# Kernel tuning notes

Measured on AMD Instinct MI355X. Metric: run time of the kernel, lower is better.

The kernel has to match this reference:

```python
import jax, jax.numpy as jnp
import numpy as np

N = 8192
IN_F = 128
OUT_F = 128


def setup_inputs() -> dict:
    key = jax.random.key(0)
    k1, k2, k3, k4 = jax.random.split(key, 4)
    h = jax.random.normal(k1, (N, IN_F), dtype=jnp.float32)
    pos = jax.random.normal(k2, (N, 1, 3), dtype=jnp.float32)
    # xavier_uniform-ish scale for params
    W = jax.random.uniform(k3, (IN_F, OUT_F), dtype=jnp.float32,
                           minval=-1.0, maxval=1.0) * (1.414 * np.sqrt(6.0 / (IN_F + OUT_F)))
    a = jax.random.uniform(k4, (2 * OUT_F + 3, 1), dtype=jnp.float32,
                           minval=-1.0, maxval=1.0) * (1.414 * np.sqrt(6.0 / (2 * OUT_F + 3 + 1)))
    return {"h": h, "pos": pos, "W": W, "a": a}


def reference(h, pos, W, a):
    # Wh: [N, F]
    Wh = h @ W
    F_ = Wh.shape[1]
    a1 = a[:F_, 0]          # weights on Wh[j] (the repeated / neighbor features)
    a2 = a[F_:2 * F_, 0]    # weights on Wh[i] (the repeat_interleaved / center features)
    a3 = a[2 * F_:, 0]      # weights on pos[i] - pos[j]
    p = pos.reshape(-1, 3)  # [N, 3]
    s_j = Wh @ a1           # [N]
    s_i = Wh @ a2           # [N]
    p_a = p @ a3            # [N]
    # e[i, j] = leaky_relu(Wh[j].a1 + Wh[i].a2 + (pos[i]-pos[j]).a3)
    e = jax.nn.leaky_relu(s_i[:, None] + s_j[None, :] + p_a[:, None] - p_a[None, :],
                          negative_slope=0.2)  # [N, N]
    attention = jax.nn.softmax(e, axis=1)
    # eval mode: dropout is identity
    h_prime = attention @ Wh  # [N, F]
    return jax.nn.elu(h_prime)
```

## Files before the change

### kernel.cpp

```cpp
#include <hip/hip_runtime.h>
#include <hip/hip_bf16.h>

#define N 8192
#define F 128
#define JC 4
#define JSLICE (N / JC)

typedef __attribute__((ext_vector_type(4)))  float f32x4;
typedef __attribute__((ext_vector_type(16))) float f32x16;
typedef __attribute__((ext_vector_type(8)))  short short8;

static __device__ __forceinline__ short bf16bits(float x) {
  __hip_bfloat16 b = __float2bfloat16(x);
  return *reinterpret_cast<short*>(&b);
}

__global__ __launch_bounds__(256) void k_gemm_cd(
    const float* __restrict__ h, const float* __restrict__ pos,
    const float* __restrict__ W, const float* __restrict__ a,
    unsigned short* __restrict__ WhTf, float* __restrict__ cArr,
    float* __restrict__ dArr)
{
  __shared__ float Ws[128 * 128];
  const int tid = threadIdx.x;
  const int r0  = blockIdx.x * 16;

  {
    f32x4* Ws4 = (f32x4*)Ws;
    const f32x4* Wg4 = (const f32x4*)W;
#pragma unroll
    for (int q = 0; q < 16; ++q) Ws4[q * 256 + tid] = Wg4[q * 256 + tid];
  }
  __syncthreads();

  const int rg  = tid >> 5;
  const int c32 = tid & 31;

  f32x4 acc0, acc1;
#pragma unroll
  for (int i = 0; i < 4; ++i) { acc0[i] = 0.0f; acc1[i] = 0.0f; }

  const f32x4* h40 = (const f32x4*)(h + (size_t)(r0 + rg * 2) * 128);
  const f32x4* h41 = (const f32x4*)(h + (size_t)(r0 + rg * 2 + 1) * 128);
  const f32x4* Ws4 = (const f32x4*)Ws;

#pragma unroll 4
  for (int k4 = 0; k4 < 32; ++k4) {
    f32x4 hv0 = h40[k4];
    f32x4 hv1 = h41[k4];
#pragma unroll
    for (int e = 0; e < 4; ++e) {
      f32x4 w = Ws4[(k4 * 4 + e) * 32 + c32];
      acc0 += hv0[e] * w;
      acc1 += hv1[e] * w;
    }
  }

  f32x4 a1v = *(const f32x4*)(a + c32 * 4);
  f32x4 a2v = *(const f32x4*)(a + 128 + c32 * 4);
#pragma unroll
  for (int rr = 0; rr < 2; ++rr) {
    f32x4 accR = rr ? acc1 : acc0;
    f32x4 t1 = accR * a1v;
    f32x4 t2 = accR * a2v;
    float s1 = t1[0] + t1[1] + t1[2] + t1[3];
    float s2 = t2[0] + t2[1] + t2[2] + t2[3];
#pragma unroll
    for (int m = 1; m < 32; m <<= 1) {
      s1 += __shfl_xor(s1, m);
      s2 += __shfl_xor(s2, m);
    }
    if (c32 == 0) {
      const int row = r0 + rg * 2 + rr;
      float pa = pos[row * 3 + 0] * a[256] + pos[row * 3 + 1] * a[257] +
                 pos[row * 3 + 2] * a[258];
      cArr[row] = s2 + pa;
      dArr[row] = s1 - pa;
    }
  }

  __syncthreads();
  float* tmp = Ws;
  {
    const int base = (rg * 2) * 132 + c32 * 4;
    *(f32x4*)&tmp[base]       = acc0;
    *(f32x4*)&tmp[base + 132] = acc1;
  }
  __syncthreads();
  {
    const int col  = tid >> 1;
    const int half = tid & 1;
    short8 o;
#pragma unroll
    for (int rr = 0; rr < 8; ++rr)
      o[rr] = bf16bits(tmp[(half * 8 + rr) * 132 + col]);
    *(short8*)(WhTf + (size_t)(r0 >> 4) * 2048 + col * 16 + half * 8) = o;
  }
}

__global__ __launch_bounds__(256, 2) void k_flash(
    const unsigned short* __restrict__ WhTf, const float* __restrict__ cArr,
    const float* __restrict__ dArr, float* __restrict__ pnum,
    float* __restrict__ pden)
{
  __shared__ __align__(16) float dS[JSLICE];
  __shared__ float redA[64 * 128];
  __shared__ float redB[64 * 128];
  __shared__ float denA[64];
  __shared__ float denB[64];

  const int tid = threadIdx.x;
  const int jc  = blockIdx.x >> 7;
  const int r0  = (blockIdx.x & 127) * 64;

  {
    const f32x4* s4 = (const f32x4*)(dArr + (size_t)jc * JSLICE);
    f32x4* t4 = (f32x4*)dS;
    t4[tid]       = s4[tid];
    t4[256 + tid] = s4[256 + tid];
  }
  __syncthreads();

  const int w  = tid >> 6;
  const int l  = tid & 63;
  const int cl = l & 31;
  const int kh = l >> 5;
  const int jw = w * (JSLICE / 4);
  const float L2E = 1.44269504f;
  const float ci0 = cArr[r0 + cl] * L2E;
  const float ci1 = cArr[r0 + 32 + cl] * L2E;

  f32x16 acc[2][4];
#pragma unroll
  for (int R = 0; R < 2; ++R)
#pragma unroll
    for (int G = 0; G < 4; ++G)
#pragma unroll
      for (int i = 0; i < 16; ++i) acc[R][G][i] = 0.0f;

  float den0 = 0.0f, den1 = 0.0f;

  const unsigned short* bPtr =
      WhTf + ((size_t)(jc * JSLICE + jw) >> 4) * 2048 + cl * 16 + kh * 8;
  const float* dPtr = dS + jw + kh * 8;

  short8 b0 = *(const short8*)(bPtr);
  short8 b1 = *(const short8*)(bPtr + 512);
  short8 b2 = *(const short8*)(bPtr + 1024);
  short8 b3 = *(const short8*)(bPtr + 1536);
  f32x4 dj0 = *(const f32x4*)(dPtr);
  f32x4 dj1 = *(const f32x4*)(dPtr + 4);
  bPtr += 2048; dPtr += 16;

  const int iters = (JSLICE / 4) / 16;
  for (int kk = 0; kk < iters; ++kk) {
    short8 n0 = *(const short8*)(bPtr);
    short8 n1 = *(const short8*)(bPtr + 512);
    short8 n2 = *(const short8*)(bPtr + 1024);
    short8 n3 = *(const short8*)(bPtr + 1536);
    f32x4 nd0 = *(const f32x4*)(dPtr);
    f32x4 nd1 = *(const f32x4*)(dPtr + 4);

    float p0[8], p1[8];
#pragma unroll
    for (int e = 0; e < 8; ++e) {
      float dj = (e < 4) ? dj0[e] : dj1[e - 4];
      float u0 = __builtin_fmaf(dj, L2E, ci0);
      u0 = fmaxf(u0, 0.2f * u0);
      float pv0 = __builtin_amdgcn_exp2f(u0);
      den0 += pv0; p0[e] = pv0;
      float u1 = __builtin_fmaf(dj, L2E, ci1);
      u1 = fmaxf(u1, 0.2f * u1);
      float pv1 = __builtin_amdgcn_exp2f(u1);
      den1 += pv1; p1[e] = pv1;
    }
    short8 af0, af1;
#pragma unroll
    for (int e = 0; e < 8; ++e) { af0[e] = bf16bits(p0[e]); af1[e] = bf16bits(p1[e]); }

    acc[0][0] = __builtin_amdgcn_mfma_f32_32x32x16_bf16(af0, b0, acc[0][0], 0, 0, 0);
    acc[1][0] = __builtin_amdgcn_mfma_f32_32x32x16_bf16(af1, b0, acc[1][0], 0, 0, 0);
    acc[0][1] = __builtin_amdgcn_mfma_f32_32x32x16_bf16(af0, b1, acc[0][1], 0, 0, 0);
    acc[1][1] = __builtin_amdgcn_mfma_f32_32x32x16_bf16(af1, b1, acc[1][1], 0, 0, 0);
    acc[0][2] = __builtin_amdgcn_mfma_f32_32x32x16_bf16(af0, b2, acc[0][2], 0, 0, 0);
    acc[1][2] = __builtin_amdgcn_mfma_f32_32x32x16_bf16(af1, b2, acc[1][2], 0, 0, 0);
    acc[0][3] = __builtin_amdgcn_mfma_f32_32x32x16_bf16(af0, b3, acc[0][3], 0, 0, 0);
    acc[1][3] = __builtin_amdgcn_mfma_f32_32x32x16_bf16(af1, b3, acc[1][3], 0, 0, 0);

    b0 = n0; b1 = n1; b2 = n2; b3 = n3;
    dj0 = nd0; dj1 = nd1;
    bPtr += 2048; dPtr += 16;
  }

  den0 += __shfl_xor(den0, 32);
  den1 += __shfl_xor(den1, 32);

  float* redW = (w & 1) ? redB : redA;
  float* denW = (w & 1) ? denB : denA;
  const int rhi = 4 * kh;
  if (w < 2) {
#pragma unroll
    for (int reg = 0; reg < 16; ++reg) {
      const int rt = (reg & 3) + 8 * (reg >> 2) + rhi;
#pragma unroll
      for (int R = 0; R < 2; ++R)
#pragma unroll
        for (int G = 0; G < 4; ++G)
          redW[(R * 32 + rt) * 128 + G * 32 + cl] = acc[R][G][reg];
    }
    if (l < 32) { denW[cl] = den0; denW[32 + cl] = den1; }
  }
  __syncthreads();
  if (w >= 2) {
#pragma unroll
    for (int reg = 0; reg < 16; ++reg) {
      const int rt = (reg & 3) + 8 * (reg >> 2) + rhi;
#pragma unroll
      for (int R = 0; R < 2; ++R)
#pragma unroll
        for (int G = 0; G < 4; ++G)
          redW[(R * 32 + rt) * 128 + G * 32 + cl] += acc[R][G][reg];
    }
    if (l < 32) { denW[cl] += den0; denW[32 + cl] += den1; }
  }
  __syncthreads();

  {
    f32x4* pn4 = (f32x4*)(pnum + (size_t)jc * N * F + (size_t)r0 * 128);
    const f32x4* rA = (const f32x4*)redA;
    const f32x4* rB = (const f32x4*)redB;
#pragma unroll
    for (int q = 0; q < 8; ++q)
      pn4[q * 256 + tid] = rA[q * 256 + tid] + rB[q * 256 + tid];
    if (tid < 64) pden[(size_t)jc * N + r0 + tid] = denA[tid] + denB[tid];
  }
}

__global__ __launch_bounds__(256) void k_final(
    const float* __restrict__ pnum, const float* __restrict__ pden,
    float* __restrict__ out)
{
  const int g = blockIdx.x * 256 + threadIdx.x;
  const int row = g >> 5;
  f32x4 n;
#pragma unroll
  for (int i = 0; i < 4; ++i) n[i] = 0.0f;
  float dd = 0.0f;
#pragma unroll
  for (int c = 0; c < JC; ++c) {
    n += ((const f32x4*)pnum)[(size_t)c * (N * F / 4) + g];
    dd += pden[(size_t)c * N + row];
  }
  f32x4 r = n * (1.0f / dd);
#pragma unroll
  for (int i = 0; i < 4; ++i) {
    float x = r[i];
    r[i] = x > 0.0f ? x : (__builtin_amdgcn_exp2f(x * 1.44269504f) - 1.0f);
  }
  ((f32x4*)out)[g] = r;
}

extern "C" void kernel_launch(void* const* d_in, const int* in_sizes, int n_in,
                              void* d_out, int out_size, void* d_ws, size_t ws_size,
                              hipStream_t stream)
{
  const float* h   = (const float*)d_in[0];
  const float* pos = (const float*)d_in[1];
  const float* W   = (const float*)d_in[2];
  const float* a   = (const float*)d_in[3];
  float* out = (float*)d_out;

  char* ws = (char*)d_ws;
  unsigned short* WhTf = (unsigned short*)ws;
  float* cArr = (float*)(ws + (size_t)2 * 1024 * 1024);
  float* dArr = cArr + N;
  float* pden = dArr + N;
  float* pnum = pden + (size_t)JC * N;

  hipLaunchKernelGGL(k_gemm_cd, dim3(512), dim3(256), 0, stream,
                     h, pos, W, a, WhTf, cArr, dArr);
  hipLaunchKernelGGL(k_flash, dim3(128 * JC), dim3(256), 0, stream,
                     WhTf, cArr, dArr, pnum, pden);
  hipLaunchKernelGGL(k_final, dim3((N * F / 4) / 256), dim3(256), 0, stream,
                     pnum, pden, out);
}
```

Before: 115.3 us.

## Split flash kernel work per wave by row tile and raise occupancy

Result: faster. 111.1 us (-3.7%).

```diff
diff --git a/kernel.cpp b/kernel.cpp
--- a/kernel.cpp
+++ b/kernel.cpp
@@ -3,7 +3,7 @@
 
 #define N 8192
 #define F 128
-#define JC 4
+#define JC 8
 #define JSLICE (N / JC)
 
 typedef __attribute__((ext_vector_type(4)))  float f32x4;
@@ -98,16 +98,14 @@
   }
 }
 
-__global__ __launch_bounds__(256, 2) void k_flash(
+__global__ __launch_bounds__(256, 4) void k_flash(
     const unsigned short* __restrict__ WhTf, const float* __restrict__ cArr,
     const float* __restrict__ dArr, float* __restrict__ pnum,
     float* __restrict__ pden)
 {
   __shared__ __align__(16) float dS[JSLICE];
-  __shared__ float redA[64 * 128];
-  __shared__ float redB[64 * 128];
-  __shared__ float denA[64];
-  __shared__ float denB[64];
+  __shared__ float red[64 * 128];
+  __shared__ float denS[64];
 
   const int tid = threadIdx.x;
   const int jc  = blockIdx.x >> 7;
@@ -115,9 +113,7 @@
 
   {
     const f32x4* s4 = (const f32x4*)(dArr + (size_t)jc * JSLICE);
-    f32x4* t4 = (f32x4*)dS;
-    t4[tid]       = s4[tid];
-    t4[256 + tid] = s4[256 + tid];
+    ((f32x4*)dS)[tid] = s4[tid];
   }
   __syncthreads();
 
@@ -125,20 +121,15 @@
   const int l  = tid & 63;
   const int cl = l & 31;
   const int kh = l >> 5;
-  const int jw = w * (JSLICE / 4);
+  const int rt = w & 1;
+  const int jw = (w >> 1) * (JSLICE / 2);
   const float L2E = 1.44269504f;
-  const float ci0 = cArr[r0 + cl] * L2E;
-  const float ci1 = cArr[r0 + 32 + cl] * L2E;
-
-  f32x16 acc[2][4];
-#pragma unroll
-  for (int R = 0; R < 2; ++R)
-#pragma unroll
-    for (int G = 0; G < 4; ++G)
-#pragma unroll
-      for (int i = 0; i < 16; ++i) acc[R][G][i] = 0.0f;
-
-  float den0 = 0.0f, den1 = 0.0f;
+  const float ci = cArr[r0 + rt * 32 + cl] * L2E;
+
+  f32x16 acc0, acc1, acc2, acc3;
+#pragma unroll
+  for (int i = 0; i < 16; ++i) { acc0[i] = 0; acc1[i] = 0; acc2[i] = 0; acc3[i] = 0; }
+  float den = 0.0f;
 
   const unsigned short* bPtr =
       WhTf + ((size_t)(jc * JSLICE + jw) >> 4) * 2048 + cl * 16 + kh * 8;
@@ -148,91 +139,72 @@
   short8 b1 = *(const short8*)(bPtr + 512);
   short8 b2 = *(const short8*)(bPtr + 1024);
   short8 b3 = *(const short8*)(bPtr + 1536);
-  f32x4 dj0 = *(const f32x4*)(dPtr);
-  f32x4 dj1 = *(const f32x4*)(dPtr + 4);
-  bPtr += 2048; dPtr += 16;
-
-  const int iters = (JSLICE / 4) / 16;
+  bPtr += 2048;
+
+  const int iters = (JSLICE / 2) / 16;
   for (int kk = 0; kk < iters; ++kk) {
     short8 n0 = *(const short8*)(bPtr);
     short8 n1 = *(const short8*)(bPtr + 512);
     short8 n2 = *(const short8*)(bPtr + 1024);
     short8 n3 = *(const short8*)(bPtr + 1536);
-    f32x4 nd0 = *(const f32x4*)(dPtr);
-    f32x4 nd1 = *(const f32x4*)(dPtr + 4);
-
-    float p0[8], p1[8];
+
+    f32x4 dj0 = *(const f32x4*)(dPtr);
+    f32x4 dj1 = *(const f32x4*)(dPtr + 4);
+    short8 af;
 #pragma unroll
     for (int e = 0; e < 8; ++e) {
       float dj = (e < 4) ? dj0[e] : dj1[e - 4];
-      float u0 = __builtin_fmaf(dj, L2E, ci0);
-      u0 = fmaxf(u0, 0.2f * u0);
-      float pv0 = __builtin_amdgcn_exp2f(u0);
-      den0 += pv0; p0[e] = pv0;
-      float u1 = __builtin_fmaf(dj, L2E, ci1);
-      u1 = fmaxf(u1, 0.2f * u1);
-      float pv1 = __builtin_amdgcn_exp2f(u1);
-      den1 += pv1; p1[e] = pv1;
-    }
-    short8 af0, af1;
-#pragma unroll
-    for (int e = 0; e < 8; ++e) { af0[e] = bf16bits(p0[e]); af1[e] = bf16bits(p1[e]); }
-
-    acc[0][0] = __builtin_amdgcn_mfma_f32_32x32x16_bf16(af0, b0, acc[0][0], 0, 0, 0);
-    acc[1][0] = __builtin_amdgcn_mfma_f32_32x32x16_bf16(af1, b0, acc[1][0], 0, 0, 0);
-    acc[0][1] = __builtin_amdgcn_mfma_f32_32x32x16_bf16(af0, b1, acc[0][1], 0, 0, 0);
-    acc[1][1] = __builtin_amdgcn_mfma_f32_32x32x16_bf16(af1, b1, acc[1][1], 0, 0, 0);
-    acc[0][2] = __builtin_amdgcn_mfma_f32_32x32x16_bf16(af0, b2, acc[0][2], 0, 0, 0);
-    acc[1][2] = __builtin_amdgcn_mfma_f32_32x32x16_bf16(af1, b2, acc[1][2], 0, 0, 0);
-    acc[0][3] = __builtin_amdgcn_mfma_f32_32x32x16_bf16(af0, b3, acc[0][3], 0, 0, 0);
-    acc[1][3] = __builtin_amdgcn_mfma_f32_32x32x16_bf16(af1, b3, acc[1][3], 0, 0, 0);
+      float u = __builtin_fmaf(dj, L2E, ci);
+      u = fmaxf(u, 0.2f * u);
+      float pv = __builtin_amdgcn_exp2f(u);
+      den += pv;
+      af[e] = bf16bits(pv);
+    }
+
+    acc0 = __builtin_amdgcn_mfma_f32_32x32x16_bf16(af, b0, acc0, 0, 0, 0);
+    acc1 = __builtin_amdgcn_mfma_f32_32x32x16_bf16(af, b1, acc1, 0, 0, 0);
+    acc2 = __builtin_amdgcn_mfma_f32_32x32x16_bf16(af, b2, acc2, 0, 0, 0);
+    acc3 = __builtin_amdgcn_mfma_f32_32x32x16_bf16(af, b3, acc3, 0, 0, 0);
 
     b0 = n0; b1 = n1; b2 = n2; b3 = n3;
-    dj0 = nd0; dj1 = nd1;
     bPtr += 2048; dPtr += 16;
   }
 
-  den0 += __shfl_xor(den0, 32);
-  den1 += __shfl_xor(den1, 32);
-
-  float* redW = (w & 1) ? redB : redA;
-  float* denW = (w & 1) ? denB : denA;
+  den += __shfl_xor(den, 32);
+
+  const int rtb = 32 * rt;
   const int rhi = 4 * kh;
   if (w < 2) {
 #pragma unroll
     for (int reg = 0; reg < 16; ++reg) {
-      const int rt = (reg & 3) + 8 * (reg >> 2) + rhi;
-#pragma unroll
-      for (int R = 0; R < 2; ++R)
-#pragma unroll
-        for (int G = 0; G < 4; ++G)
-          redW[(R * 32 + rt) * 128 + G * 32 + cl] = acc[R][G][reg];
-    }
-    if (l < 32) { denW[cl] = den0; denW[32 + cl] = den1; }
+      const int rr = (reg & 3) + 8 * (reg >> 2) + rhi;
+      red[(rtb + rr) * 128 +  0 + cl] = acc0[reg];
+      red[(rtb + rr) * 128 + 32 + cl] = acc1[reg];
+      red[(rtb + rr) * 128 + 64 + cl] = acc2[reg];
+      red[(rtb + rr) * 128 + 96 + cl] = acc3[reg];
+    }
+    if (l < 32) denS[rtb + l] = den;
   }
   __syncthreads();
   if (w >= 2) {
 #pragma unroll
     for (int reg = 0; reg < 16; ++reg) {
-      const int rt = (reg & 3) + 8 * (reg >> 2) + rhi;
-#pragma unroll
-      for (int R = 0; R < 2; ++R)
-#pragma unroll
-        for (int G = 0; G < 4; ++G)
-          redW[(R * 32 + rt) * 128 + G * 32 + cl] += acc[R][G][reg];
-    }
-    if (l < 32) { denW[cl] += den0; denW[32 + cl] += den1; }
+      const int rr = (reg & 3) + 8 * (reg >> 2) + rhi;
+      red[(rtb + rr) * 128 +  0 + cl] += acc0[reg];
+      red[(rtb + rr) * 128 + 32 + cl] += acc1[reg];
+      red[(rtb + rr) * 128 + 64 + cl] += acc2[reg];
+      red[(rtb + rr) * 128 + 96 + cl] += acc3[reg];
+    }
+    if (l < 32) denS[rtb + l] += den;
   }
   __syncthreads();
 
   {
     f32x4* pn4 = (f32x4*)(pnum + (size_t)jc * N * F + (size_t)r0 * 128);
-    const f32x4* rA = (const f32x4*)redA;
-    const f32x4* rB = (const f32x4*)redB;
-#pragma unroll
-    for (int q = 0; q < 8; ++q)
-      pn4[q * 256 + tid] = rA[q * 256 + tid] + rB[q * 256 + tid];
-    if (tid < 64) pden[(size_t)jc * N + r0 + tid] = denA[tid] + denB[tid];
+    const f32x4* r4 = (const f32x4*)red;
+#pragma unroll
+    for (int q = 0; q < 8; ++q) pn4[q * 256 + tid] = r4[q * 256 + tid];
+    if (tid < 64) pden[(size_t)jc * N + r0 + tid] = denS[tid];
   }
 }
 
```
